# Performance work log

Measured on AMD Instinct MI355X. Metric: run time of the kernel, lower is better.

Reference implementation:

```python
import jax, jax.numpy as jnp
import numpy as np

N_HEADS = 16
ROPE_BASE = 10000.0


def _apply_rope(t, cos, sin):
    # t: (B, H, S, D); cos/sin: (S, D/2). Rotate-half convention.
    d2 = t.shape[-1] // 2
    t1, t2 = t[..., :d2], t[..., d2:]
    return jnp.concatenate([t1 * cos - t2 * sin, t2 * cos + t1 * sin], axis=-1)


def setup_inputs() -> dict:
    key = jax.random.key(0)
    k0, k1, k2, k3, k4 = jax.random.split(key, 5)
    B, S, E = 4, 2048, 1024
    scale = 0.02
    x = jax.random.normal(k0, (B, S, E), dtype=jnp.float32)
    w_qkv = jax.random.normal(k1, (E, 3 * E), dtype=jnp.float32) * scale
    b_qkv = jnp.zeros((3 * E,), dtype=jnp.float32)
    w_proj = jax.random.normal(k2, (E, E), dtype=jnp.float32) * scale
    b_proj = jnp.zeros((E,), dtype=jnp.float32)
    return {"x": x, "w_qkv": w_qkv, "b_qkv": b_qkv, "w_proj": w_proj, "b_proj": b_proj}


def reference(x, w_qkv, b_qkv, w_proj, b_proj):
    B, S, E = x.shape
    H = N_HEADS
    D = E // H
    # fused QKV projection
    qkv = x @ w_qkv + b_qkv                      # (B, S, 3E)
    q, k, v = jnp.split(qkv, 3, axis=-1)
    def to_heads(t):
        return t.reshape(B, S, H, D).transpose(0, 2, 1, 3)  # (B, H, S, D)
    q, k, v = to_heads(q), to_heads(k), to_heads(v)
    # RoPE (rotate-half)
    inv_freq = ROPE_BASE ** (-jnp.arange(0, D, 2, dtype=jnp.float32) / D)  # (D/2,)
    pos = jnp.arange(S, dtype=jnp.float32)
    freqs = pos[:, None] * inv_freq[None, :]     # (S, D/2)
    cos, sin = jnp.cos(freqs), jnp.sin(freqs)
    q = _apply_rope(q, cos, sin)
    k = _apply_rope(k, cos, sin)
    # causal SDPA
    scores = jnp.einsum('bhqd,bhkd->bhqk', q, k) / jnp.sqrt(jnp.float32(D))
    causal = jnp.tril(jnp.ones((S, S), dtype=bool))
    scores = jnp.where(causal, scores, jnp.float32(-1e30))
    probs = jax.nn.softmax(scores, axis=-1)
    out = jnp.einsum('bhqk,bhkd->bhqd', probs, v)  # (B, H, S, D)
    out = out.transpose(0, 2, 1, 3).reshape(B, S, E)
    # output projection (dropout is identity at p=0 / eval)
    return out @ w_proj + b_proj
```

## Files before the change

### kernel.cpp

```cpp
#include <hip/hip_runtime.h>

typedef unsigned short u16;
typedef __bf16 bf16x8 __attribute__((ext_vector_type(8)));
typedef float f32x4 __attribute__((ext_vector_type(4)));

__device__ __forceinline__ u16 f2b(float f) {
    unsigned u = __builtin_bit_cast(unsigned, f);
    unsigned r = (u + 0x7fffu + ((u >> 16) & 1u)) >> 16;
    return (u16)r;
}
#if __has_builtin(__builtin_amdgcn_cvt_pk_bf16_f32)
typedef __bf16 bf16x2_t __attribute__((ext_vector_type(2)));
__device__ __forceinline__ unsigned pk2(float a, float b) {
    return __builtin_bit_cast(unsigned, __builtin_amdgcn_cvt_pk_bf16_f32(a, b));
}
#else
__device__ __forceinline__ unsigned pk2(float a, float b) {
    return (unsigned)f2b(a) | ((unsigned)f2b(b) << 16);
}
#endif
#if __has_builtin(__builtin_amdgcn_exp2f)
#define EXP2F(x) __builtin_amdgcn_exp2f(x)
#else
#define EXP2F(x) exp2f(x)
#endif

__device__ __forceinline__ void gl_lds16(const u16* g, u16* l) {
    __builtin_amdgcn_global_load_lds(
        (const __attribute__((address_space(1))) unsigned*)(const void*)g,
        (__attribute__((address_space(3))) unsigned*)(void*)l, 16, 0, 0);
}

__global__ __launch_bounds__(256) void k_convert(const float* __restrict__ in,
                                                 u16* __restrict__ out, int n8) {
    int i = blockIdx.x * 256 + threadIdx.x;
    if (i >= n8) return;
    const float4* p = (const float4*)(in + (size_t)i * 8);
    float4 a = p[0], b = p[1];
    u16 t[8] = {f2b(a.x), f2b(a.y), f2b(a.z), f2b(a.w),
                f2b(b.x), f2b(b.y), f2b(b.z), f2b(b.w)};
    *(uint4*)(out + (size_t)i * 8) = *(const uint4*)t;
}

__global__ __launch_bounds__(256) void k_transpose_bf16(const float* __restrict__ in,
                                                        u16* __restrict__ out,
                                                        int R, int C) {
    __shared__ u16 tile[64][72];
    int tc = blockIdx.x * 64;
    int tr = blockIdx.y * 64;
    for (int i = threadIdx.x; i < 4096; i += 256) {
        int r = i >> 6, c = i & 63;
        tile[c][r] = f2b(in[(size_t)(tr + r) * C + tc + c]);
    }
    __syncthreads();
    for (int i = threadIdx.x; i < 4096; i += 256) {
        int r = i >> 6, c = i & 63;
        out[(size_t)(tc + r) * R + tr + c] = tile[r][c];
    }
}

__device__ __forceinline__ void gemm_mainloop(const u16* __restrict__ Ab,
                                              const u16* __restrict__ Bb, int K,
                                              u16* As, u16* Bs, int tid,
                                              f32x4 (&acc)[4][4]) {
    const int wave = tid >> 6, lane = tid & 63;
    const int col = lane & 15, quad = lane >> 4;
    const int wm = wave >> 1, wn = wave & 1;
    const int lrow = lane >> 2, lk = (lane & 3) * 8;
    u16* ldsA0 = As + (wave * 16) * 32;
    u16* ldsA1 = As + (64 + wave * 16) * 32;
    u16* ldsB0 = Bs + (wave * 16) * 32;
    u16* ldsB1 = Bs + (64 + wave * 16) * 32;
    const u16* gA0 = Ab + (size_t)(wave * 16 + lrow) * K + lk;
    const u16* gA1 = gA0 + (size_t)64 * K;
    const u16* gB0 = Bb + (size_t)(wave * 16 + lrow) * K + lk;
    const u16* gB1 = gB0 + (size_t)64 * K;
    for (int k0 = 0; k0 < K; k0 += 32) {
        if (k0) __syncthreads();
        gl_lds16(gA0 + k0, ldsA0);
        gl_lds16(gA1 + k0, ldsA1);
        gl_lds16(gB0 + k0, ldsB0);
        gl_lds16(gB1 + k0, ldsB1);
        __syncthreads();
        bf16x8 af[4], bfr[4];
#pragma unroll
        for (int mt = 0; mt < 4; ++mt)
            af[mt] = *(const bf16x8*)(As + (wm * 64 + mt * 16 + col) * 32 + quad * 8);
#pragma unroll
        for (int nt = 0; nt < 4; ++nt)
            bfr[nt] = *(const bf16x8*)(Bs + (wn * 64 + nt * 16 + col) * 32 + quad * 8);
#pragma unroll
        for (int mt = 0; mt < 4; ++mt)
#pragma unroll
            for (int nt = 0; nt < 4; ++nt)
                acc[mt][nt] = __builtin_amdgcn_mfma_f32_16x16x32_bf16(
                    af[mt], bfr[nt], acc[mt][nt], 0, 0, 0);
    }
}

__global__ __launch_bounds__(256) void k_gemm_qkv_rope(
    const u16* __restrict__ A, const u16* __restrict__ Bt,
    const float* __restrict__ bias, u16* __restrict__ Qr, u16* __restrict__ Kr,
    u16* __restrict__ Vt) {
    __shared__ __align__(16) u16 As[128 * 32];
    __shared__ __align__(16) u16 Bs[128 * 32];
    const int K = 1024;
    int tid = threadIdx.x;
    int lane = tid & 63, wave = tid >> 6;
    int col = lane & 15, quad = lane >> 4;
    int wm = wave >> 1, wn = wave & 1;
    int mBase = blockIdx.y * 128;
    int nBase = blockIdx.x * 128;
    f32x4 acc[4][4] = {};
    gemm_mainloop(A + (size_t)mBase * K, Bt + (size_t)nBase * K, K, As, Bs, tid, acc);

    int n64 = nBase + wn * 64;
    int region = n64 >> 10;
    int h = (n64 & 1023) >> 6;
    if (region < 2) {
        u16* out = (region == 0) ? Qr : Kr;
        float qs = (region == 0) ? 0.18033688011112042f : 1.0f;
        const float C0 = 0.4152410118609203f;
#pragma unroll
        for (int nt = 0; nt < 2; ++nt) {
            int d1 = nt * 16 + col;
            float inv_freq = exp2f(-C0 * (float)d1);
            float b1 = bias[n64 + nt * 16 + col];
            float b2 = bias[n64 + nt * 16 + col + 32];
#pragma unroll
            for (int mt = 0; mt < 4; ++mt) {
                int mrow = mBase + wm * 64 + mt * 16 + quad * 4;
#pragma unroll
                for (int r = 0; r < 4; ++r) {
                    int m = mrow + r;
                    int s = m & 2047, b = m >> 11;
                    float sn, cs;
                    sincosf((float)s * inv_freq, &sn, &cs);
                    float t1 = acc[mt][nt][r] + b1;
                    float t2 = acc[mt][nt + 2][r] + b2;
                    size_t base = ((size_t)((b * 16 + h) * 2048 + s)) * 64;
                    out[base + d1] = f2b((t1 * cs - t2 * sn) * qs);
                    out[base + d1 + 32] = f2b((t2 * cs + t1 * sn) * qs);
                }
            }
        }
    } else {
#pragma unroll
        for (int nt = 0; nt < 4; ++nt) {
            int d = nt * 16 + col;
            float bv = bias[n64 + nt * 16 + col];
#pragma unroll
            for (int mt = 0; mt < 4; ++mt) {
                int mrow = mBase + wm * 64 + mt * 16 + quad * 4;
#pragma unroll
                for (int r = 0; r < 4; ++r) {
                    int m = mrow + r;
                    int s = m & 2047, b = m >> 11;
                    Vt[((size_t)((b * 16 + h) * 64 + d)) * 2048 + s] =
                        f2b(acc[mt][nt][r] + bv);
                }
            }
        }
    }
}

__global__ __launch_bounds__(256) void k_attn(const u16* __restrict__ Qr,
                                              const u16* __restrict__ Kr,
                                              const u16* __restrict__ Vt,
                                              u16* __restrict__ O) {
    __shared__ __align__(16) u16 Ks[64 * 72];
    __shared__ __align__(16) u16 Vs[64 * 72];
    int tid = threadIdx.x, wave = tid >> 6, lane = tid & 63;
    int col = lane & 15, quad = lane >> 4;
    int bx = blockIdx.x, bh = blockIdx.y;
    int b = bh >> 4, h = bh & 15;
    size_t headQ = (size_t)bh * 2048 * 64;
    size_t headV = (size_t)bh * 64 * 2048;
    int r0 = tid >> 3, kc = tid & 7;
    int rb72 = ((col >> 2) * 8 + (col & 3)) * 72;

    for (int half = 0; half < 2; ++half) {
        int qt = half ? bx : (31 - bx);
        int myq = qt * 64 + wave * 16 + col;
        const u16* qptr = Qr + headQ + (size_t)myq * 64;
        bf16x8 aq0 = *(const bf16x8*)(qptr + quad * 8);
        bf16x8 aq1 = *(const bf16x8*)(qptr + 32 + quad * 8);
        f32x4 o[4] = {};
        float l = 0.f;

        for (int j = 0; j <= qt; ++j) {
            __syncthreads();
            {
                const u16* kg = Kr + headQ + (size_t)(j * 64 + r0) * 64 + kc * 8;
                const u16* vg = Vt + headV + (size_t)r0 * 2048 + j * 64 + kc * 8;
                *(uint4*)(Ks + r0 * 72 + kc * 8) = *(const uint4*)kg;
                *(uint4*)(Ks + (r0 + 32) * 72 + kc * 8) = *(const uint4*)(kg + 32 * 64);
                *(uint4*)(Vs + r0 * 72 + kc * 8) = *(const uint4*)vg;
                *(uint4*)(Vs + (r0 + 32) * 72 + kc * 8) = *(const uint4*)(vg + 32 * 2048);
            }
            __syncthreads();
            f32x4 s[4];
#pragma unroll
            for (int nt = 0; nt < 4; ++nt) {
                const u16* kp = Ks + rb72 + ((nt & 1) * 32 + (nt >> 1) * 4) * 72;
                bf16x8 ak0 = *(const bf16x8*)(kp + quad * 8);
                bf16x8 ak1 = *(const bf16x8*)(kp + 32 + quad * 8);
                f32x4 z = {};
                z = __builtin_amdgcn_mfma_f32_16x16x32_bf16(ak0, aq0, z, 0, 0, 0);
                s[nt] = __builtin_amdgcn_mfma_f32_16x16x32_bf16(ak1, aq1, z, 0, 0, 0);
            }
            if (j == qt) {
#pragma unroll
                for (int nt = 0; nt < 4; ++nt) {
                    int keyb = qt * 64 + (nt & 1) * 32 + quad * 8 + (nt >> 1) * 4;
#pragma unroll
                    for (int r = 0; r < 4; ++r)
                        if (keyb + r > myq) s[nt][r] = -3.0e38f;
                }
            }
            unsigned P4[8];
#pragma unroll
            for (int nt = 0; nt < 4; ++nt) {
                float p0 = EXP2F(s[nt][0]);
                float p1 = EXP2F(s[nt][1]);
                float p2 = EXP2F(s[nt][2]);
                float p3 = EXP2F(s[nt][3]);
                l += (p0 + p1) + (p2 + p3);
                P4[2 * nt] = pk2(p0, p1);
                P4[2 * nt + 1] = pk2(p2, p3);
            }
#pragma unroll
            for (int kk = 0; kk < 2; ++kk) {
                uint4 bw;
                bw.x = P4[2 * kk];
                bw.y = P4[2 * kk + 1];
                bw.z = P4[2 * kk + 4];
                bw.w = P4[2 * kk + 5];
                bf16x8 bp = __builtin_bit_cast(bf16x8, bw);
#pragma unroll
                for (int mt = 0; mt < 4; ++mt) {
                    bf16x8 av = *(const bf16x8*)(Vs + (mt * 16 + col) * 72 + kk * 32 + quad * 8);
                    o[mt] = __builtin_amdgcn_mfma_f32_16x16x32_bf16(av, bp, o[mt], 0, 0, 0);
                }
            }
        }
        l += __shfl_xor(l, 16);
        l += __shfl_xor(l, 32);
        float inv = 1.0f / l;
        u16* orow = O + (size_t)(b * 2048 + myq) * 1024 + h * 64;
#pragma unroll
        for (int mt = 0; mt < 4; ++mt) {
            uint2 w;
            w.x = pk2(o[mt][0] * inv, o[mt][1] * inv);
            w.y = pk2(o[mt][2] * inv, o[mt][3] * inv);
            *(uint2*)(orow + mt * 16 + quad * 4) = w;
        }
    }
}

__global__ __launch_bounds__(256) void k_gemm_proj(const u16* __restrict__ A,
                                                   const u16* __restrict__ Bt,
                                                   const float* __restrict__ bias,
                                                   float* __restrict__ out) {
    __shared__ __align__(16) u16 As[128 * 32];
    __shared__ __align__(16) u16 Bs[128 * 32];
    const int K = 1024;
    int tid = threadIdx.x;
    int lane = tid & 63, wave = tid >> 6;
    int col = lane & 15, quad = lane >> 4;
    int wm = wave >> 1, wn = wave & 1;
    int mBase = blockIdx.y * 128;
    int nBase = blockIdx.x * 128;
    f32x4 acc[4][4] = {};
    gemm_mainloop(A + (size_t)mBase * K, Bt + (size_t)nBase * K, K, As, Bs, tid, acc);
#pragma unroll
    for (int nt = 0; nt < 4; ++nt) {
        int n = nBase + wn * 64 + nt * 16 + col;
        float bv = bias[n];
#pragma unroll
        for (int mt = 0; mt < 4; ++mt) {
            int m = mBase + wm * 64 + mt * 16 + quad * 4;
#pragma unroll
            for (int r = 0; r < 4; ++r)
                out[(size_t)(m + r) * 1024 + n] = acc[mt][nt][r] + bv;
        }
    }
}

extern "C" void kernel_launch(void* const* d_in, const int* in_sizes, int n_in,
                              void* d_out, int out_size, void* d_ws, size_t ws_size,
                              hipStream_t stream) {
    const float* x = (const float*)d_in[0];
    const float* w_qkv = (const float*)d_in[1];
    const float* b_qkv = (const float*)d_in[2];
    const float* w_proj = (const float*)d_in[3];
    const float* b_proj = (const float*)d_in[4];
    float* out = (float*)d_out;
    char* ws = (char*)d_ws;
    u16* x_bf = (u16*)(ws);
    u16* wqkvT = (u16*)(ws + 16777216);
    u16* wprojT = (u16*)(ws + 23068672);
    u16* Qr = (u16*)(ws + 25165824);
    u16* Kr = (u16*)(ws + 41943040);
    u16* Vt = (u16*)(ws + 58720256);
    u16* AO = (u16*)(ws + 75497472);

    k_convert<<<4096, 256, 0, stream>>>(x, x_bf, 1048576);
    k_transpose_bf16<<<dim3(48, 16), 256, 0, stream>>>(w_qkv, wqkvT, 1024, 3072);
    k_transpose_bf16<<<dim3(16, 16), 256, 0, stream>>>(w_proj, wprojT, 1024, 1024);
    k_gemm_qkv_rope<<<dim3(24, 64), 256, 0, stream>>>(x_bf, wqkvT, b_qkv, Qr, Kr, Vt);
    k_attn<<<dim3(16, 64), 256, 0, stream>>>(Qr, Kr, Vt, AO);
    k_gemm_proj<<<dim3(8, 64), 256, 0, stream>>>(AO, wprojT, b_proj, out);
}
```

Baseline: 299.1 us.

## Process two query tiles per wave in attention and double GEMM k-step

The attention kernel now has each block handle two adjacent 64-row query tiles, so every K/V tile staged in LDS serves both, halving K/V global loads and barriers per query. The grid is halved to match, with balanced pairing of early and late query blocks kept. The GEMM main loop now loads 64 k-columns per barrier pair instead of 32, doubling LDS tiles to cut synchronisation overhead. The costs are more registers (two sets of accumulators), fewer attention blocks to fill the GPU, and a doubled LDS footprint in the GEMMs.

```diff
diff --git a/kernel.cpp b/kernel.cpp
--- a/kernel.cpp
+++ b/kernel.cpp
@@ -75,26 +75,35 @@
     const u16* gA1 = gA0 + (size_t)64 * K;
     const u16* gB0 = Bb + (size_t)(wave * 16 + lrow) * K + lk;
     const u16* gB1 = gB0 + (size_t)64 * K;
-    for (int k0 = 0; k0 < K; k0 += 32) {
+    for (int k0 = 0; k0 < K; k0 += 64) {
         if (k0) __syncthreads();
-        gl_lds16(gA0 + k0, ldsA0);
-        gl_lds16(gA1 + k0, ldsA1);
-        gl_lds16(gB0 + k0, ldsB0);
-        gl_lds16(gB1 + k0, ldsB1);
+#pragma unroll
+        for (int kh = 0; kh < 2; ++kh) {
+            int ko = k0 + kh * 32;
+            gl_lds16(gA0 + ko, ldsA0 + kh * 4096);
+            gl_lds16(gA1 + ko, ldsA1 + kh * 4096);
+            gl_lds16(gB0 + ko, ldsB0 + kh * 4096);
+            gl_lds16(gB1 + ko, ldsB1 + kh * 4096);
+        }
         __syncthreads();
-        bf16x8 af[4], bfr[4];
-#pragma unroll
-        for (int mt = 0; mt < 4; ++mt)
-            af[mt] = *(const bf16x8*)(As + (wm * 64 + mt * 16 + col) * 32 + quad * 8);
-#pragma unroll
-        for (int nt = 0; nt < 4; ++nt)
-            bfr[nt] = *(const bf16x8*)(Bs + (wn * 64 + nt * 16 + col) * 32 + quad * 8);
-#pragma unroll
-        for (int mt = 0; mt < 4; ++mt)
+#pragma unroll
+        for (int kh = 0; kh < 2; ++kh) {
+            bf16x8 af[4], bfr[4];
+#pragma unroll
+            for (int mt = 0; mt < 4; ++mt)
+                af[mt] = *(const bf16x8*)(As + kh * 4096 +
+                                          (wm * 64 + mt * 16 + col) * 32 + quad * 8);
 #pragma unroll
             for (int nt = 0; nt < 4; ++nt)
-                acc[mt][nt] = __builtin_amdgcn_mfma_f32_16x16x32_bf16(
-                    af[mt], bfr[nt], acc[mt][nt], 0, 0, 0);
+                bfr[nt] = *(const bf16x8*)(Bs + kh * 4096 +
+                                           (wn * 64 + nt * 16 + col) * 32 + quad * 8);
+#pragma unroll
+            for (int mt = 0; mt < 4; ++mt)
+#pragma unroll
+                for (int nt = 0; nt < 4; ++nt)
+                    acc[mt][nt] = __builtin_amdgcn_mfma_f32_16x16x32_bf16(
+                        af[mt], bfr[nt], acc[mt][nt], 0, 0, 0);
+        }
     }
 }
 
@@ -102,8 +111,8 @@
     const u16* __restrict__ A, const u16* __restrict__ Bt,
     const float* __restrict__ bias, u16* __restrict__ Qr, u16* __restrict__ Kr,
     u16* __restrict__ Vt) {
-    __shared__ __align__(16) u16 As[128 * 32];
-    __shared__ __align__(16) u16 Bs[128 * 32];
+    __shared__ __align__(16) u16 As[2 * 128 * 32];
+    __shared__ __align__(16) u16 Bs[2 * 128 * 32];
     const int K = 1024;
     int tid = threadIdx.x;
     int lane = tid & 63, wave = tid >> 6;
@@ -180,15 +189,21 @@
     int rb72 = ((col >> 2) * 8 + (col & 3)) * 72;
 
     for (int half = 0; half < 2; ++half) {
-        int qt = half ? bx : (31 - bx);
-        int myq = qt * 64 + wave * 16 + col;
-        const u16* qptr = Qr + headQ + (size_t)myq * 64;
-        bf16x8 aq0 = *(const bf16x8*)(qptr + quad * 8);
-        bf16x8 aq1 = *(const bf16x8*)(qptr + 32 + quad * 8);
-        f32x4 o[4] = {};
-        float l = 0.f;
-
-        for (int j = 0; j <= qt; ++j) {
+        int qb = half ? bx : (15 - bx);
+        int t0 = 2 * qb, t1 = t0 + 1;
+        int myq0 = qb * 128 + wave * 16 + col;
+        int myq1 = myq0 + 64;
+        const u16* qp0 = Qr + headQ + (size_t)myq0 * 64;
+        const u16* qp1 = Qr + headQ + (size_t)myq1 * 64;
+        bf16x8 aq00 = *(const bf16x8*)(qp0 + quad * 8);
+        bf16x8 aq01 = *(const bf16x8*)(qp0 + 32 + quad * 8);
+        bf16x8 aq10 = *(const bf16x8*)(qp1 + quad * 8);
+        bf16x8 aq11 = *(const bf16x8*)(qp1 + 32 + quad * 8);
+        f32x4 o0[4] = {}, o1[4] = {};
+        float l0 = 0.f, l1 = 0.f;
+
+        for (int j = 0; j <= t1; ++j) {
+            bool d0 = (j <= t0);
             __syncthreads();
             {
                 const u16* kg = Kr + headQ + (size_t)(j * 64 + r0) * 64 + kc * 8;
@@ -199,61 +214,100 @@
                 *(uint4*)(Vs + (r0 + 32) * 72 + kc * 8) = *(const uint4*)(vg + 32 * 2048);
             }
             __syncthreads();
-            f32x4 s[4];
+            f32x4 s0[4], s1[4];
 #pragma unroll
             for (int nt = 0; nt < 4; ++nt) {
                 const u16* kp = Ks + rb72 + ((nt & 1) * 32 + (nt >> 1) * 4) * 72;
                 bf16x8 ak0 = *(const bf16x8*)(kp + quad * 8);
                 bf16x8 ak1 = *(const bf16x8*)(kp + 32 + quad * 8);
+                if (d0) {
+                    f32x4 z = {};
+                    z = __builtin_amdgcn_mfma_f32_16x16x32_bf16(ak0, aq00, z, 0, 0, 0);
+                    s0[nt] = __builtin_amdgcn_mfma_f32_16x16x32_bf16(ak1, aq01, z, 0, 0, 0);
+                }
                 f32x4 z = {};
-                z = __builtin_amdgcn_mfma_f32_16x16x32_bf16(ak0, aq0, z, 0, 0, 0);
-                s[nt] = __builtin_amdgcn_mfma_f32_16x16x32_bf16(ak1, aq1, z, 0, 0, 0);
-            }
-            if (j == qt) {
+                z = __builtin_amdgcn_mfma_f32_16x16x32_bf16(ak0, aq10, z, 0, 0, 0);
+                s1[nt] = __builtin_amdgcn_mfma_f32_16x16x32_bf16(ak1, aq11, z, 0, 0, 0);
+            }
+            if (j == t0) {
 #pragma unroll
                 for (int nt = 0; nt < 4; ++nt) {
-                    int keyb = qt * 64 + (nt & 1) * 32 + quad * 8 + (nt >> 1) * 4;
+                    int keyb = j * 64 + (nt & 1) * 32 + quad * 8 + (nt >> 1) * 4;
 #pragma unroll
                     for (int r = 0; r < 4; ++r)
-                        if (keyb + r > myq) s[nt][r] = -3.0e38f;
-                }
-            }
-            unsigned P4[8];
+                        if (keyb + r > myq0) s0[nt][r] = -3.0e38f;
+                }
+            }
+            if (j == t1) {
+#pragma unroll
+                for (int nt = 0; nt < 4; ++nt) {
+                    int keyb = j * 64 + (nt & 1) * 32 + quad * 8 + (nt >> 1) * 4;
+#pragma unroll
+                    for (int r = 0; r < 4; ++r)
+                        if (keyb + r > myq1) s1[nt][r] = -3.0e38f;
+                }
+            }
+            unsigned P40[8], P41[8];
+            if (d0) {
+#pragma unroll
+                for (int nt = 0; nt < 4; ++nt) {
+                    float p0 = EXP2F(s0[nt][0]);
+                    float p1 = EXP2F(s0[nt][1]);
+                    float p2 = EXP2F(s0[nt][2]);
+                    float p3 = EXP2F(s0[nt][3]);
+                    l0 += (p0 + p1) + (p2 + p3);
+                    P40[2 * nt] = pk2(p0, p1);
+                    P40[2 * nt + 1] = pk2(p2, p3);
+                }
+            }
 #pragma unroll
             for (int nt = 0; nt < 4; ++nt) {
-                float p0 = EXP2F(s[nt][0]);
-                float p1 = EXP2F(s[nt][1]);
-                float p2 = EXP2F(s[nt][2]);
-                float p3 = EXP2F(s[nt][3]);
-                l += (p0 + p1) + (p2 + p3);
-                P4[2 * nt] = pk2(p0, p1);
-                P4[2 * nt + 1] = pk2(p2, p3);
+                float p0 = EXP2F(s1[nt][0]);
+                float p1 = EXP2F(s1[nt][1]);
+                float p2 = EXP2F(s1[nt][2]);
+                float p3 = EXP2F(s1[nt][3]);
+                l1 += (p0 + p1) + (p2 + p3);
+                P41[2 * nt] = pk2(p0, p1);
+                P41[2 * nt + 1] = pk2(p2, p3);
             }
 #pragma unroll
             for (int kk = 0; kk < 2; ++kk) {
-                uint4 bw;
-                bw.x = P4[2 * kk];
-                bw.y = P4[2 * kk + 1];
-                bw.z = P4[2 * kk + 4];
-                bw.w = P4[2 * kk + 5];
-                bf16x8 bp = __builtin_bit_cast(bf16x8, bw);
+                uint4 bw0, bw1;
+                bw0.x = P40[2 * kk];
+                bw0.y = P40[2 * kk + 1];
+                bw0.z = P40[2 * kk + 4];
+                bw0.w = P40[2 * kk + 5];
+                bw1.x = P41[2 * kk];
+                bw1.y = P41[2 * kk + 1];
+                bw1.z = P41[2 * kk + 4];
+                bw1.w = P41[2 * kk + 5];
+                bf16x8 bp0 = __builtin_bit_cast(bf16x8, bw0);
+                bf16x8 bp1 = __builtin_bit_cast(bf16x8, bw1);
 #pragma unroll
                 for (int mt = 0; mt < 4; ++mt) {
                     bf16x8 av = *(const bf16x8*)(Vs + (mt * 16 + col) * 72 + kk * 32 + quad * 8);
-                    o[mt] = __builtin_amdgcn_mfma_f32_16x16x32_bf16(av, bp, o[mt], 0, 0, 0);
-                }
-            }
-        }
-        l += __shfl_xor(l, 16);
-        l += __shfl_xor(l, 32);
-        float inv = 1.0f / l;
-        u16* orow = O + (size_t)(b * 2048 + myq) * 1024 + h * 64;
+                    if (d0)
+                        o0[mt] = __builtin_amdgcn_mfma_f32_16x16x32_bf16(av, bp0, o0[mt], 0, 0, 0);
+                    o1[mt] = __builtin_amdgcn_mfma_f32_16x16x32_bf16(av, bp1, o1[mt], 0, 0, 0);
+                }
+            }
+        }
+        l0 += __shfl_xor(l0, 16);
+        l0 += __shfl_xor(l0, 32);
+        l1 += __shfl_xor(l1, 16);
+        l1 += __shfl_xor(l1, 32);
+        float inv0 = 1.0f / l0, inv1 = 1.0f / l1;
+        u16* orow0 = O + (size_t)(b * 2048 + myq0) * 1024 + h * 64;
+        u16* orow1 = O + (size_t)(b * 2048 + myq1) * 1024 + h * 64;
 #pragma unroll
         for (int mt = 0; mt < 4; ++mt) {
-            uint2 w;
-            w.x = pk2(o[mt][0] * inv, o[mt][1] * inv);
-            w.y = pk2(o[mt][2] * inv, o[mt][3] * inv);
-            *(uint2*)(orow + mt * 16 + quad * 4) = w;
+            uint2 w0, w1;
+            w0.x = pk2(o0[mt][0] * inv0, o0[mt][1] * inv0);
+            w0.y = pk2(o0[mt][2] * inv0, o0[mt][3] * inv0);
+            w1.x = pk2(o1[mt][0] * inv1, o1[mt][1] * inv1);
+            w1.y = pk2(o1[mt][2] * inv1, o1[mt][3] * inv1);
+            *(uint2*)(orow0 + mt * 16 + quad * 4) = w0;
+            *(uint2*)(orow1 + mt * 16 + quad * 4) = w1;
         }
     }
 }
@@ -262,8 +316,8 @@
                                                    const u16* __restrict__ Bt,
                                                    const float* __restrict__ bias,
                                                    float* __restrict__ out) {
-    __shared__ __align__(16) u16 As[128 * 32];
-    __shared__ __align__(16) u16 Bs[128 * 32];
+    __shared__ __align__(16) u16 As[2 * 128 * 32];
+    __shared__ __align__(16) u16 Bs[2 * 128 * 32];
     const int K = 1024;
     int tid = threadIdx.x;
     int lane = tid & 63, wave = tid >> 6;
@@ -309,6 +363,6 @@
     k_transpose_bf16<<<dim3(48, 16), 256, 0, stream>>>(w_qkv, wqkvT, 1024, 3072);
     k_transpose_bf16<<<dim3(16, 16), 256, 0, stream>>>(w_proj, wprojT, 1024, 1024);
     k_gemm_qkv_rope<<<dim3(24, 64), 256, 0, stream>>>(x_bf, wqkvT, b_qkv, Qr, Kr, Vt);
-    k_attn<<<dim3(16, 64), 256, 0, stream>>>(Qr, Kr, Vt, AO);
+    k_attn<<<dim3(8, 64), 256, 0, stream>>>(Qr, Kr, Vt, AO);
     k_gemm_proj<<<dim3(8, 64), 256, 0, stream>>>(AO, wprojT, b_proj, out);
 }
```

Result: faster. 278.1 us (-7.0%).
